# Performance work log

Hardware: AMD Instinct MI355X
Metric: run time of the kernel (lower is better)

Reference implementation:

```python
import jax, jax.numpy as jnp
import numpy as np

B, L, M, D, H, FF, W = 2, 2048, 2048, 1024, 16, 4096, 64
DH = D // H


def _layernorm(x, g, b, eps=1e-5):
    mu = x.mean(-1, keepdims=True)
    var = ((x - mu) ** 2).mean(-1, keepdims=True)
    return (x - mu) / jnp.sqrt(var + eps) * g + b


def _mha(qx, kx, wq, bq, wk, bk, wv, bv, wo, bo, mask, bias):
    Bq, Lq, _ = qx.shape
    Lk = kx.shape[1]
    q = (qx @ wq + bq).reshape(Bq, Lq, H, DH).transpose(0, 2, 1, 3)  # [B,H,Lq,DH]
    k = (kx @ wk + bk).reshape(Bq, Lk, H, DH).transpose(0, 2, 1, 3)
    v = (kx @ wv + bv).reshape(Bq, Lk, H, DH).transpose(0, 2, 1, 3)
    s = jnp.einsum('bhqd,bhkd->bhqk', q, k) / jnp.sqrt(jnp.asarray(DH, qx.dtype))
    if bias is not None:
        s = s + bias[None]  # bias: [H,Lq,Lk]
    if mask is not None:
        s = jnp.where(mask[None, None], s, jnp.asarray(-1e9, qx.dtype))
    a = jax.nn.softmax(s, axis=-1)
    o = jnp.einsum('bhqk,bhkd->bhqd', a, v).transpose(0, 2, 1, 3).reshape(Bq, Lq, D)
    return o @ wo + bo


def _forward(x, mem,
             swq, sbq, swk, sbk, swv, sbv, swo, sbo,
             cwq, cbq, cwk, cbk, cwv, cbv, cwo, cbo,
             w1, b1, w2, b2,
             g1, be1, g2, be2, g3, be3):
    i = jnp.arange(L)[:, None]
    j = jnp.arange(L)[None, :]
    # causal local window mask: attend to j<=i with i-j < W
    mask = (j <= i) & ((i - j) < W)
    # ALiBi slopes for power-of-2 head counts: 2^{-8h/H}, h=1..H
    slopes = (2.0 ** (-8.0 * jnp.arange(1, H + 1, dtype=x.dtype) / H))
    bias = slopes[:, None, None] * (j - i).astype(x.dtype)[None]  # [H,L,L], <=0 on causal part
    sa = _mha(x, x, swq, sbq, swk, sbk, swv, sbv, swo, sbo, mask, bias)
    x = _layernorm(x + sa, g1, be1)
    # cross-attn mask is all ones -> no masking, no bias
    ca = _mha(x, mem, cwq, cbq, cwk, cbk, cwv, cbv, cwo, cbo, None, None)
    x = _layernorm(x + ca, g2, be2)
    ff = jax.nn.gelu(x @ w1 + b1, approximate=False) @ w2 + b2
    return _layernorm(x + ff, g3, be3)


def setup_inputs() -> dict:
    key = jax.random.key(0)
    ks = jax.random.split(key, 16)
    s = 0.02
    inp = {
        'x': jax.random.normal(ks[0], (B, L, D), jnp.float32),
        'mem': jax.random.normal(ks[1], (B, M, D), jnp.float32),
    }
    # self-attn params
    for n, k in zip(['swq', 'swk', 'swv', 'swo'], jax.random.split(ks[2], 4)):
        inp[n] = jax.random.normal(k, (D, D), jnp.float32) * s
    for n in ['sbq', 'sbk', 'sbv', 'sbo']:
        inp[n] = jnp.zeros((D,), jnp.float32)
    # cross-attn params
    for n, k in zip(['cwq', 'cwk', 'cwv', 'cwo'], jax.random.split(ks[3], 4)):
        inp[n] = jax.random.normal(k, (D, D), jnp.float32) * s
    for n in ['cbq', 'cbk', 'cbv', 'cbo']:
        inp[n] = jnp.zeros((D,), jnp.float32)
    # FFN params
    inp['w1'] = jax.random.normal(ks[4], (D, FF), jnp.float32) * s
    inp['b1'] = jnp.zeros((FF,), jnp.float32)
    inp['w2'] = jax.random.normal(ks[5], (FF, D), jnp.float32) * s
    inp['b2'] = jnp.zeros((D,), jnp.float32)
    # LayerNorm params
    for n in ['g1', 'g2', 'g3']:
        inp[n] = jnp.ones((D,), jnp.float32)
    for n in ['be1', 'be2', 'be3']:
        inp[n] = jnp.zeros((D,), jnp.float32)
    return inp


def reference(x, mem,
              swq, sbq, swk, sbk, swv, sbv, swo, sbo,
              cwq, cbq, cwk, cbk, cwv, cbv, cwo, cbo,
              w1, b1, w2, b2,
              g1, be1, g2, be2, g3, be3):
    return _forward(x, mem,
                    swq, sbq, swk, sbk, swv, sbv, swo, sbo,
                    cwq, cbq, cwk, cbk, cwv, cbv, cwo, cbo,
                    w1, b1, w2, b2,
                    g1, be1, g2, be2, g3, be3)
```

## Files before the change

### kernel.cpp

```cpp
#include <hip/hip_runtime.h>
#include <hip/hip_bf16.h>
#include <math.h>

#define Bc 2
#define Lc 2048
#define Mc 2048
#define Dc 1024
#define Hc 16
#define FFc 4096
#define DHc 64

typedef __bf16 bf16;
typedef float f32x4 __attribute__((ext_vector_type(4)));
typedef __bf16 bf16x8 __attribute__((ext_vector_type(8)));
typedef __bf16 bf16x4 __attribute__((ext_vector_type(4)));
typedef __bf16 bf16x2 __attribute__((ext_vector_type(2)));

struct Ptrs8 { const float* p[8]; };

__device__ inline void gload16(const bf16* g, const bf16* lds_base) {
  __builtin_amdgcn_global_load_lds(
      (const __attribute__((address_space(1))) void*)g,
      (__attribute__((address_space(3))) void*)lds_base, 16, 0, 0);
}

#define WAIT_VM(n) asm volatile("s_waitcnt vmcnt(" #n ")" ::: "memory")
#define WAIT_LGKM(n) asm volatile("s_waitcnt lgkmcnt(" #n ")" ::: "memory")
#define RAW_BAR() __builtin_amdgcn_s_barrier()
#define SCHED_FENCE() __builtin_amdgcn_sched_barrier(0)

__device__ inline float gelu_f(float v) {
  float u = 0.7978845608f * (v + 0.044715f * v * v * v);
  float e = exp2f(u * 2.885390082f);
  float th = 1.0f - 2.0f / (e + 1.0f);
  return 0.5f * v * (1.0f + th);
}

__device__ inline int xcd_remap(int flat, int nwg) {
  int cpx = nwg >> 3;
  return (flat & 7) * cpx + (flat >> 3);
}

__global__ __launch_bounds__(256) void k_f2b(const float* __restrict__ in,
                                             bf16* __restrict__ out, long n4) {
  long i = (long)blockIdx.x * 256 + threadIdx.x;
  if (i >= n4) return;
  f32x4 v = *(const f32x4*)(in + i * 4);
  bf16x4 o;
  o[0] = (bf16)v[0]; o[1] = (bf16)v[1]; o[2] = (bf16)v[2]; o[3] = (bf16)v[3];
  *(bf16x4*)(out + i * 4) = o;
}

__global__ __launch_bounds__(256) void k_transpose_w8(Ptrs8 srcs,
                                                      bf16* __restrict__ out) {
  __shared__ float tile[64][65];
  const float* in = srcs.p[blockIdx.z];
  bf16* o = out + (long)blockIdx.z * Dc * Dc;
  int n0 = blockIdx.x * 64, k0 = blockIdx.y * 64;
  int t = threadIdx.x;
  int tr = t >> 4, tc = (t & 15) * 4;
#pragma unroll
  for (int p = 0; p < 4; p++) {
    int r = p * 16 + tr;
    f32x4 v = *(const f32x4*)(in + (long)(k0 + r) * Dc + n0 + tc);
    tile[r][tc] = v[0]; tile[r][tc + 1] = v[1];
    tile[r][tc + 2] = v[2]; tile[r][tc + 3] = v[3];
  }
  __syncthreads();
#pragma unroll
  for (int p = 0; p < 4; p++) {
    int rn = p * 16 + tr;
    bf16x4 ov;
    ov[0] = (bf16)tile[tc + 0][rn]; ov[1] = (bf16)tile[tc + 1][rn];
    ov[2] = (bf16)tile[tc + 2][rn]; ov[3] = (bf16)tile[tc + 3][rn];
    *(bf16x4*)(o + (long)(n0 + rn) * Dc + k0 + tc) = ov;
  }
}

__global__ __launch_bounds__(256) void k_transpose_w(const float* __restrict__ in,
                                                     bf16* __restrict__ out,
                                                     int K, int N) {
  __shared__ float tile[64][65];
  int n0 = blockIdx.x * 64, k0 = blockIdx.y * 64;
  int t = threadIdx.x;
  int tr = t >> 4, tc = (t & 15) * 4;
#pragma unroll
  for (int p = 0; p < 4; p++) {
    int r = p * 16 + tr;
    f32x4 v = *(const f32x4*)(in + (long)(k0 + r) * N + n0 + tc);
    tile[r][tc] = v[0]; tile[r][tc + 1] = v[1];
    tile[r][tc + 2] = v[2]; tile[r][tc + 3] = v[3];
  }
  __syncthreads();
#pragma unroll
  for (int p = 0; p < 4; p++) {
    int rn = p * 16 + tr;
    bf16x4 o;
    o[0] = (bf16)tile[tc + 0][rn]; o[1] = (bf16)tile[tc + 1][rn];
    o[2] = (bf16)tile[tc + 2][rn]; o[3] = (bf16)tile[tc + 3][rn];
    *(bf16x4*)(out + (long)(n0 + rn) * K + k0 + tc) = o;
  }
}

__global__ __launch_bounds__(256) void k_transpose_v(const bf16* __restrict__ vb,
                                                     bf16* __restrict__ vt, int N) {
  __shared__ bf16 tile[64][72];
  int j0 = blockIdx.x * 64;
  int bh = blockIdx.y; int b = bh >> 4; int h = bh & 15;
  int t = threadIdx.x;
#pragma unroll
  for (int c = 0; c < 2; c++) {
    int id = t + c * 256;
    int r = id >> 3, c8 = (id & 7) * 8;
    *(bf16x8*)&tile[r][c8] =
        *(const bf16x8*)(vb + ((long)(b * N + j0 + r)) * Dc + h * DHc + c8);
  }
  __syncthreads();
#pragma unroll
  for (int c = 0; c < 2; c++) {
    int id = t + c * 256;
    int d = id >> 3, j8 = (id & 7) * 8;
    bf16x8 o;
#pragma unroll
    for (int e = 0; e < 8; e++) o[e] = tile[j8 + e][d];
    *(bf16x8*)(vt + ((long)bh * DHc + d) * N + j0 + j8) = o;
  }
}

__global__ __launch_bounds__(256) void k_gemm128(
    const bf16* __restrict__ A0, const bf16* __restrict__ A1,
    const bf16* __restrict__ A2, long lda,
    const bf16* __restrict__ B0, long bstride,
    bf16* __restrict__ outB, long ldc, long cstride,
    const float* __restrict__ bias0, const float* __restrict__ bias1,
    const float* __restrict__ bias2, int Kdim, int act, float scale0) {
  __shared__ __align__(16) bf16 As[2][128 * 64];
  __shared__ __align__(16) bf16 Bs[2][128 * 64];
  int gx = gridDim.x, gy = gridDim.y;
  int nwg = gx * gy * gridDim.z;
  int flat = (blockIdx.z * gy + blockIdx.y) * gx + blockIdx.x;
  int f2 = xcd_remap(flat, nwg);
  int bxi = f2 % gx; int tmp = f2 / gx;
  int byi = tmp % gy; int z = tmp / gy;
  const bf16* A = (z == 0) ? A0 : ((z == 1) ? A1 : A2);
  const bf16* Bt = B0 + (long)z * bstride;
  const float* bias = (z == 0) ? bias0 : ((z == 1) ? bias1 : bias2);
  float scl = (z == 0) ? scale0 : 1.0f;
  long cbase = (long)z * cstride;
  int bm = byi * 128, bn = bxi * 128;
  int t = threadIdx.x, w = t >> 6, lane = t & 63;
  int wm = w >> 1, wn = w & 1;
  int lr = lane & 15, lg = lane >> 4;
  int srow = lane >> 3;
  int scol = (((lane & 7) * 16) ^ ((lane >> 3) << 4)) >> 1;
  f32x4 acc[4][4] = {};
  int nk = Kdim >> 6;
  auto stage = [&](int buf, int kt2) {
    long k0 = (long)kt2 * 64;
#pragma unroll
    for (int i = 0; i < 4; i++) {
      int row = (i * 4 + w) * 8 + srow;
      gload16(A + (long)(bm + row) * lda + k0 + scol, &As[buf][(i * 4 + w) * 512]);
      gload16(Bt + (long)(bn + row) * Kdim + k0 + scol, &Bs[buf][(i * 4 + w) * 512]);
    }
  };
  stage(0, 0);
  if (nk > 1) stage(1, 1);
  for (int kt = 0; kt < nk; ++kt) {
    int cur = kt & 1;
    if (kt + 1 < nk) { WAIT_VM(8); } else { WAIT_VM(0); }
    RAW_BAR();
    SCHED_FENCE();
    const char* pa = (const char*)&As[cur][0];
    const char* pb = (const char*)&Bs[cur][0];
    int xr = (lr & 7) << 4;
    bf16x8 af[2][4], bfr[2][4];
#pragma unroll
    for (int m = 0; m < 4; m++) {
      int row = wm * 64 + m * 16 + lr;
      af[0][m] = *(const bf16x8*)(pa + (row << 7) + ((lg * 16) ^ xr));
    }
#pragma unroll
    for (int n = 0; n < 4; n++) {
      int row = wn * 64 + n * 16 + lr;
      bfr[0][n] = *(const bf16x8*)(pb + (row << 7) + ((lg * 16) ^ xr));
    }
    SCHED_FENCE();
#pragma unroll
    for (int m = 0; m < 4; m++) {
      int row = wm * 64 + m * 16 + lr;
      af[1][m] = *(const bf16x8*)(pa + (row << 7) + ((64 + lg * 16) ^ xr));
    }
#pragma unroll
    for (int n = 0; n < 4; n++) {
      int row = wn * 64 + n * 16 + lr;
      bfr[1][n] = *(const bf16x8*)(pb + (row << 7) + ((64 + lg * 16) ^ xr));
    }
    SCHED_FENCE();
    WAIT_LGKM(8);
    SCHED_FENCE();
#pragma unroll
    for (int m = 0; m < 4; m++)
#pragma unroll
      for (int n = 0; n < 4; n++)
        acc[m][n] = __builtin_amdgcn_mfma_f32_16x16x32_bf16(af[0][m], bfr[0][n],
                                                            acc[m][n], 0, 0, 0);
    WAIT_LGKM(0);
    SCHED_FENCE();
    RAW_BAR();
    if (kt + 2 < nk) stage(cur, kt + 2);
    SCHED_FENCE();
#pragma unroll
    for (int m = 0; m < 4; m++)
#pragma unroll
      for (int n = 0; n < 4; n++)
        acc[m][n] = __builtin_amdgcn_mfma_f32_16x16x32_bf16(af[1][m], bfr[1][n],
                                                            acc[m][n], 0, 0, 0);
  }
#pragma unroll
  for (int n = 0; n < 4; n++) {
    int cg = bn + wn * 64 + n * 16 + lr;
    float bv = bias ? bias[cg] : 0.0f;
#pragma unroll
    for (int m = 0; m < 4; m++) {
#pragma unroll
      for (int rr = 0; rr < 4; rr++) {
        int rg = bm + wm * 64 + m * 16 + lg * 4 + rr;
        float v = (acc[m][n][rr] + bv) * scl;
        if (act == 1) v = gelu_f(v);
        outB[cbase + (long)rg * ldc + cg] = (bf16)v;
      }
    }
  }
}

__global__ __launch_bounds__(256) void k_gemmsk(
    const bf16* __restrict__ A, long lda,
    const bf16* __restrict__ Bt, int Kfull,
    float* __restrict__ psum, long slab, int Kchunk, int ldc) {
  __shared__ __align__(16) bf16 As[2][128 * 64];
  __shared__ __align__(16) bf16 Bs[2][128 * 64];
  int gx = gridDim.x, gy = gridDim.y;
  int nwg = gx * gy * gridDim.z;
  int flat = (blockIdx.z * gy + blockIdx.y) * gx + blockIdx.x;
  int f2 = xcd_remap(flat, nwg);
  int bxi = f2 % gx; int tmp = f2 / gx;
  int byi = tmp % gy; int z = tmp / gy;
  int bm = byi * 128, bn = bxi * 128;
  int t = threadIdx.x, w = t >> 6, lane = t & 63;
  int wm = w >> 1, wn = w & 1;
  int lr = lane & 15, lg = lane >> 4;
  int srow = lane >> 3;
  int scol = (((lane & 7) * 16) ^ ((lane >> 3) << 4)) >> 1;
  f32x4 acc[4][4] = {};
  int nk = Kchunk >> 6;
  long kstart = (long)z * Kchunk;
  auto stage = [&](int buf, int kt2) {
    long k0 = kstart + (long)kt2 * 64;
#pragma unroll
    for (int i = 0; i < 4; i++) {
      int row = (i * 4 + w) * 8 + srow;
      gload16(A + (long)(bm + row) * lda + k0 + scol, &As[buf][(i * 4 + w) * 512]);
      gload16(Bt + (long)(bn + row) * Kfull + k0 + scol, &Bs[buf][(i * 4 + w) * 512]);
    }
  };
  stage(0, 0);
  if (nk > 1) stage(1, 1);
  for (int kt = 0; kt < nk; ++kt) {
    int cur = kt & 1;
    if (kt + 1 < nk) { WAIT_VM(8); } else { WAIT_VM(0); }
    RAW_BAR();
    SCHED_FENCE();
    const char* pa = (const char*)&As[cur][0];
    const char* pb = (const char*)&Bs[cur][0];
    int xr = (lr & 7) << 4;
    bf16x8 af[2][4], bfr[2][4];
#pragma unroll
    for (int m = 0; m < 4; m++) {
      int row = wm * 64 + m * 16 + lr;
      af[0][m] = *(const bf16x8*)(pa + (row << 7) + ((lg * 16) ^ xr));
    }
#pragma unroll
    for (int n = 0; n < 4; n++) {
      int row = wn * 64 + n * 16 + lr;
      bfr[0][n] = *(const bf16x8*)(pb + (row << 7) + ((lg * 16) ^ xr));
    }
    SCHED_FENCE();
#pragma unroll
    for (int m = 0; m < 4; m++) {
      int row = wm * 64 + m * 16 + lr;
      af[1][m] = *(const bf16x8*)(pa + (row << 7) + ((64 + lg * 16) ^ xr));
    }
#pragma unroll
    for (int n = 0; n < 4; n++) {
      int row = wn * 64 + n * 16 + lr;
      bfr[1][n] = *(const bf16x8*)(pb + (row << 7) + ((64 + lg * 16) ^ xr));
    }
    SCHED_FENCE();
    WAIT_LGKM(8);
    SCHED_FENCE();
#pragma unroll
    for (int m = 0; m < 4; m++)
#pragma unroll
      for (int n = 0; n < 4; n++)
        acc[m][n] = __builtin_amdgcn_mfma_f32_16x16x32_bf16(af[0][m], bfr[0][n],
                                                            acc[m][n], 0, 0, 0);
    WAIT_LGKM(0);
    SCHED_FENCE();
    RAW_BAR();
    if (kt + 2 < nk) stage(cur, kt + 2);
    SCHED_FENCE();
#pragma unroll
    for (int m = 0; m < 4; m++)
#pragma unroll
      for (int n = 0; n < 4; n++)
        acc[m][n] = __builtin_amdgcn_mfma_f32_16x16x32_bf16(af[1][m], bfr[1][n],
                                                            acc[m][n], 0, 0, 0);
  }
  float* po = psum + (long)z * slab;
#pragma unroll
  for (int n = 0; n < 4; n++) {
    int cg = bn + wn * 64 + n * 16 + lr;
#pragma unroll
    for (int m = 0; m < 4; m++) {
#pragma unroll
      for (int rr = 0; rr < 4; rr++) {
        int rg = bm + wm * 64 + m * 16 + lg * 4 + rr;
        po[(long)rg * ldc + cg] = acc[m][n][rr];
      }
    }
  }
}

template <int WINDOWED>
__global__ __launch_bounds__(256) void k_flash(const bf16* __restrict__ Qg,
                                               const bf16* __restrict__ Kg,
                                               const bf16* __restrict__ Vtg,
                                               bf16* __restrict__ Og, int nkv) {
  __shared__ __align__(16) bf16 Qs[64 * 64];
  __shared__ __align__(16) bf16 Ks[2][64 * 64];
  __shared__ __align__(16) bf16 Vs[2][64 * 64];
  int flat = blockIdx.y * 32 + blockIdx.x;
  int flat2 = (flat & 7) * 128 + (flat >> 3);
  int i0 = (flat2 & 31) * 64;
  int bh = flat2 >> 5;
  int b = bh >> 4, h = bh & 15;
  int t = threadIdx.x, w = t >> 6, lane = t & 63;
  int lr = lane & 15, lg = lane >> 4;
  long qoff = ((long)b * Lc + i0) * Dc + h * DHc;
  long koff = ((long)b * nkv) * Dc + h * DHc;
  long vtoff = (long)bh * DHc * nkv;
  int o0 = w * 1024 + (lane << 4), o1 = o0 + 4096;
  int r0 = o0 >> 7, c0 = (o0 & 127) ^ ((r0 & 7) << 4);
  int r1 = o1 >> 7, c1 = (o1 & 127) ^ ((r1 & 7) << 4);
  int d0 = c0 >> 1, d1 = c1 >> 1;
  gload16(Qg + qoff + (long)r0 * Dc + d0, &Qs[w * 512]);
  gload16(Qg + qoff + (long)r1 * Dc + d1, &Qs[2048 + w * 512]);
  int kb0 = WINDOWED ? (i0 >= 64 ? i0 - 64 : 0) : 0;
  int nt = WINDOWED ? ((i0 - kb0) >> 6) + 1 : (nkv >> 6);
  auto stage = [&](int buf, int kbase) {
    gload16(Kg + koff + (long)(kbase + r0) * Dc + d0, &Ks[buf][w * 512]);
    gload16(Kg + koff + (long)(kbase + r1) * Dc + d1, &Ks[buf][2048 + w * 512]);
    gload16(Vtg + vtoff + (long)r0 * nkv + kbase + d0, &Vs[buf][w * 512]);
    gload16(Vtg + vtoff + (long)r1 * nkv + kbase + d1, &Vs[buf][2048 + w * 512]);
  };
  stage(0, kb0);
  WAIT_VM(4);
  RAW_BAR();
  SCHED_FENCE();
  bf16x8 bq[2];
#pragma unroll
  for (int ks = 0; ks < 2; ks++) {
    int rq = w * 16 + lr, cb = ks * 64 + lg * 16;
    bq[ks] = *(const bf16x8*)&Qs[((rq << 7) + (cb ^ ((rq & 7) << 4))) >> 1];
  }
  char* pbase = (char*)&Qs[w * 1024];
  float mrun = -1e30f, lrun = 0.f;
  f32x4 oa[4] = {};
  float slopeL2 = WINDOWED ? exp2f(-0.5f * (float)(h + 1)) * 1.44269504f : 0.0f;
  int qabs = i0 + w * 16 + lr;
  for (int tch = 0; tch < nt; tch++) {
    int cur = tch & 1;
    if (tch + 1 < nt) {
      stage(cur ^ 1, kb0 + (tch + 1) * 64);
      WAIT_VM(4);
    } else {
      WAIT_VM(0);
    }
    RAW_BAR();
    SCHED_FENCE();
    int kbase = kb0 + tch * 64;
    f32x4 st[4] = {};
    __builtin_amdgcn_s_setprio(1);
#pragma unroll
    for (int ks = 0; ks < 2; ks++) {
#pragma unroll
      for (int m = 0; m < 4; m++) {
        int rk = m * 16 + lr, cb = ks * 64 + lg * 16;
        bf16x8 ka = *(const bf16x8*)&Ks[cur][((rk << 7) + (cb ^ ((rk & 7) << 4))) >> 1];
        st[m] = __builtin_amdgcn_mfma_f32_16x16x32_bf16(ka, bq[ks], st[m], 0, 0, 0);
      }
    }
    __builtin_amdgcn_s_setprio(0);
    float sc[4][4];
#pragma unroll
    for (int m = 0; m < 4; m++)
#pragma unroll
      for (int rr = 0; rr < 4; rr++) {
        float v = st[m][rr];
        if (WINDOWED) {
          int kab = kbase + m * 16 + lg * 4 + rr;
          v += slopeL2 * (float)(kab - qabs);
          bool valid = (kab <= qabs) && (qabs - kab < 64);
          v = valid ? v : -3.0e38f;
        }
        sc[m][rr] = v;
      }
    float pmax = fmaxf(fmaxf(sc[0][0], sc[0][1]), sc[0][2]);
    pmax = fmaxf(fmaxf(pmax, sc[0][3]), sc[1][0]);
    pmax = fmaxf(fmaxf(pmax, sc[1][1]), sc[1][2]);
    pmax = fmaxf(fmaxf(pmax, sc[1][3]), sc[2][0]);
    pmax = fmaxf(fmaxf(pmax, sc[2][1]), sc[2][2]);
    pmax = fmaxf(fmaxf(pmax, sc[2][3]), sc[3][0]);
    pmax = fmaxf(fmaxf(pmax, sc[3][1]), sc[3][2]);
    pmax = fmaxf(pmax, sc[3][3]);
    pmax = fmaxf(pmax, __shfl_xor(pmax, 16));
    pmax = fmaxf(pmax, __shfl_xor(pmax, 32));
    float mx = mrun;
    if (!__all(pmax - mrun <= 8.0f)) {
      mx = fmaxf(mrun, pmax);
      float corr = exp2f(mrun - mx);
      mrun = mx;
      lrun *= corr;
      float cq[4];
#pragma unroll
      for (int rr = 0; rr < 4; rr++) cq[rr] = __shfl(corr, lg * 4 + rr);
#pragma unroll
      for (int jd = 0; jd < 4; jd++) {
        oa[jd][0] *= cq[0]; oa[jd][1] *= cq[1];
        oa[jd][2] *= cq[2]; oa[jd][3] *= cq[3];
      }
    }
    float ps0 = 0.f, ps1 = 0.f;
#pragma unroll
    for (int m = 0; m < 4; m++) {
#pragma unroll
      for (int hh = 0; hh < 2; hh++) {
        float p0 = exp2f(sc[m][2 * hh] - mx);
        float p1 = exp2f(sc[m][2 * hh + 1] - mx);
        ps0 += p0; ps1 += p1;
        bf16x2 pw; pw[0] = (bf16)p0; pw[1] = (bf16)p1;
        int kcol = m * 16 + lg * 4 + 2 * hh;
        *(bf16x2*)(pbase + (lr << 7) + (((kcol << 1)) ^ ((lr & 7) << 4))) = pw;
      }
    }
    lrun += ps0 + ps1;
    __builtin_amdgcn_s_setprio(1);
#pragma unroll
    for (int ks = 0; ks < 2; ks++) {
      bf16x8 pa = *(const bf16x8*)(pbase + (lr << 7) +
                                   (((ks * 64 + lg * 16)) ^ ((lr & 7) << 4)));
#pragma unroll
      for (int jd = 0; jd < 4; jd++) {
        int rv = jd * 16 + lr, cb = ks * 64 + lg * 16;
        bf16x8 vf = *(const bf16x8*)&Vs[cur][((rv << 7) + (cb ^ ((rv & 7) << 4))) >> 1];
        oa[jd] = __builtin_amdgcn_mfma_f32_16x16x32_bf16(pa, vf, oa[jd], 0, 0, 0);
      }
    }
    __builtin_amdgcn_s_setprio(0);
    WAIT_LGKM(0);
    SCHED_FENCE();
    RAW_BAR();
  }
  float ls = lrun + __shfl_xor(lrun, 16);
  ls += __shfl_xor(ls, 32);
  float inv = 1.0f / ls;
  float iq[4];
#pragma unroll
  for (int rr = 0; rr < 4; rr++) iq[rr] = __shfl(inv, lg * 4 + rr);
#pragma unroll
  for (int rr = 0; rr < 4; rr++) {
    int qo = i0 + w * 16 + lg * 4 + rr;
#pragma unroll
    for (int jd = 0; jd < 4; jd++)
      Og[((long)b * Lc + qo) * Dc + h * DHc + jd * 16 + lr] =
          (bf16)(oa[jd][rr] * iq[rr]);
  }
}

template <int NS>
__global__ __launch_bounds__(256) void k_lnred(const float* __restrict__ psum,
                                               long slab,
                                               const float* __restrict__ bias,
                                               const float* __restrict__ addsrc,
                                               const float* __restrict__ g,
                                               const float* __restrict__ bb,
                                               float* __restrict__ outF,
                                               bf16* __restrict__ outB) {
  long row = blockIdx.x;
  int t = threadIdx.x; int lane = t & 63; int wid = t >> 6;
  __shared__ float red[8];
  f32x4 v = *(const f32x4*)(psum + row * Dc + t * 4);
#pragma unroll
  for (int s = 1; s < NS; s++) {
    f32x4 u = *(const f32x4*)(psum + s * slab + row * Dc + t * 4);
    v[0] += u[0]; v[1] += u[1]; v[2] += u[2]; v[3] += u[3];
  }
  f32x4 bv = *(const f32x4*)(bias + t * 4);
  f32x4 av = *(const f32x4*)(addsrc + row * Dc + t * 4);
  v[0] += bv[0] + av[0]; v[1] += bv[1] + av[1];
  v[2] += bv[2] + av[2]; v[3] += bv[3] + av[3];
  float s = v[0] + v[1] + v[2] + v[3];
  float s2 = v[0] * v[0] + v[1] * v[1] + v[2] * v[2] + v[3] * v[3];
#pragma unroll
  for (int off = 1; off < 64; off <<= 1) {
    s += __shfl_xor(s, off);
    s2 += __shfl_xor(s2, off);
  }
  if (lane == 0) { red[wid] = s; red[4 + wid] = s2; }
  __syncthreads();
  s = red[0] + red[1] + red[2] + red[3];
  s2 = red[4] + red[5] + red[6] + red[7];
  float mu = s * (1.0f / Dc);
  float var = s2 * (1.0f / Dc) - mu * mu;
  float rs = rsqrtf(var + 1e-5f);
#pragma unroll
  for (int e = 0; e < 4; e++) {
    int c = t * 4 + e;
    float y = (v[e] - mu) * rs * g[c] + bb[c];
    if (outF) outF[row * Dc + c] = y;
    if (outB) outB[row * Dc + c] = (bf16)y;
  }
}

extern "C" void kernel_launch(void* const* d_in, const int* in_sizes, int n_in,
                              void* d_out, int out_size, void* d_ws,
                              size_t ws_size, hipStream_t stream) {
  (void)in_sizes; (void)n_in; (void)out_size; (void)ws_size;
  const float* x = (const float*)d_in[0];
  const float* mem = (const float*)d_in[1];
  const float* swq = (const float*)d_in[2];
  const float* swk = (const float*)d_in[3];
  const float* swv = (const float*)d_in[4];
  const float* swo = (const float*)d_in[5];
  const float* sbq = (const float*)d_in[6];
  const float* sbk = (const float*)d_in[7];
  const float* sbv = (const float*)d_in[8];
  const float* sbo = (const float*)d_in[9];
  const float* cwq = (const float*)d_in[10];
  const float* cwk = (const float*)d_in[11];
  const float* cwv = (const float*)d_in[12];
  const float* cwo = (const float*)d_in[13];
  const float* cbq = (const float*)d_in[14];
  const float* cbk = (const float*)d_in[15];
  const float* cbv = (const float*)d_in[16];
  const float* cbo = (const float*)d_in[17];
  const float* w1 = (const float*)d_in[18];
  const float* b1 = (const float*)d_in[19];
  const float* w2 = (const float*)d_in[20];
  const float* b2 = (const float*)d_in[21];
  const float* g1 = (const float*)d_in[22];
  const float* g2 = (const float*)d_in[23];
  const float* g3 = (const float*)d_in[24];
  const float* be1 = (const float*)d_in[25];
  const float* be2 = (const float*)d_in[26];
  const float* be3 = (const float*)d_in[27];
  float* out = (float*)d_out;

  char* ws = (char*)d_ws;
  size_t off = 0;
  auto alloc = [&](size_t bytes) -> char* {
    char* p = ws + off;
    off = (off + bytes + 255) & ~(size_t)255;
    return p;
  };

  const long BL = (long)Bc * Lc;
  const long BM = (long)Bc * Mc;
  const long DD = (long)Dc * Dc;
  const long SL = BL * Dc;
  const float QSCL = 0.125f * 1.44269504f;

  bf16* wT0 = (bf16*)alloc((size_t)8 * DD * 2);
  bf16* w1T = (bf16*)alloc((size_t)FFc * Dc * 2);
  bf16* w2T = (bf16*)alloc((size_t)Dc * FFc * 2);
  bf16* xb = (bf16*)alloc((size_t)BL * Dc * 2);
  bf16* memb = (bf16*)alloc((size_t)BM * Dc * 2);
  bf16* x1b = (bf16*)alloc((size_t)BL * Dc * 2);
  bf16* x2b = (bf16*)alloc((size_t)BL * Dc * 2);
  bf16* qb = (bf16*)alloc((size_t)BL * Dc * 2);
  bf16* kb = (bf16*)alloc((size_t)BM * Dc * 2);
  bf16* vb = (bf16*)alloc((size_t)BM * Dc * 2);
  bf16* ob = (bf16*)alloc((size_t)BL * Dc * 2);
  bf16* vtS = (bf16*)alloc((size_t)Bc * Hc * DHc * Lc * 2);
  bf16* vtC = (bf16*)alloc((size_t)Bc * Hc * DHc * Mc * 2);
  float* x1f = (float*)alloc((size_t)BL * Dc * 4);
  float* x2f = (float*)alloc((size_t)BL * Dc * 4);
  bf16* ffh = (bf16*)alloc((size_t)BL * FFc * 2);
  float* psum = (float*)alloc((size_t)4 * SL * 4);

  Ptrs8 srcs;
  srcs.p[0] = swq; srcs.p[1] = swk; srcs.p[2] = swv; srcs.p[3] = swo;
  srcs.p[4] = cwq; srcs.p[5] = cwk; srcs.p[6] = cwv; srcs.p[7] = cwo;
  k_transpose_w8<<<dim3(Dc / 64, Dc / 64, 8), 256, 0, stream>>>(srcs, wT0);
  k_transpose_w<<<dim3(FFc / 64, Dc / 64), 256, 0, stream>>>(w1, w1T, Dc, FFc);
  k_transpose_w<<<dim3(Dc / 64, FFc / 64), 256, 0, stream>>>(w2, w2T, FFc, Dc);
  k_f2b<<<dim3((unsigned)(BL * Dc / 4 / 256)), 256, 0, stream>>>(x, xb, BL * Dc / 4);
  k_f2b<<<dim3((unsigned)(BM * Dc / 4 / 256)), 256, 0, stream>>>(mem, memb, BM * Dc / 4);

  k_gemm128<<<dim3(Dc / 128, BL / 128, 3), 256, 0, stream>>>(
      xb, xb, xb, Dc, wT0, DD, qb, Dc, SL, sbq, sbk, sbv, Dc, 0, QSCL);
  k_transpose_v<<<dim3(Lc / 64, Bc * Hc), 256, 0, stream>>>(vb, vtS, Lc);
  k_flash<1><<<dim3(Lc / 64, Bc * Hc), 256, 0, stream>>>(qb, kb, vtS, ob, Lc);
  k_gemmsk<<<dim3(Dc / 128, BL / 128, 2), 256, 0, stream>>>(
      ob, Dc, wT0 + 3 * DD, Dc, psum, SL, 512, Dc);
  k_lnred<2><<<dim3((unsigned)BL), 256, 0, stream>>>(psum, SL, sbo, x, g1, be1,
                                                     x1f, x1b);

  k_gemm128<<<dim3(Dc / 128, BM / 128, 3), 256, 0, stream>>>(
      x1b, memb, memb, Dc, wT0 + 4 * DD, DD, qb, Dc, SL, cbq, cbk, cbv, Dc, 0, QSCL);
  k_transpose_v<<<dim3(Mc / 64, Bc * Hc), 256, 0, stream>>>(vb, vtC, Mc);
  k_flash<0><<<dim3(Lc / 64, Bc * Hc), 256, 0, stream>>>(qb, kb, vtC, ob, Mc);
  k_gemmsk<<<dim3(Dc / 128, BL / 128, 2), 256, 0, stream>>>(
      ob, Dc, wT0 + 7 * DD, Dc, psum, SL, 512, Dc);
  k_lnred<2><<<dim3((unsigned)BL), 256, 0, stream>>>(psum, SL, cbo, x1f, g2, be2,
                                                     x2f, x2b);

  k_gemm128<<<dim3(FFc / 128, BL / 128, 1), 256, 0, stream>>>(
      x2b, x2b, x2b, Dc, w1T, 0, ffh, FFc, 0, b1, b1, b1, Dc, 1, 1.0f);
  k_gemmsk<<<dim3(Dc / 128, BL / 128, 4), 256, 0, stream>>>(
      ffh, FFc, w2T, FFc, psum, SL, 1024, Dc);
  k_lnred<4><<<dim3((unsigned)BL), 256, 0, stream>>>(psum, SL, b2, x2f, g3, be3,
                                                     out, nullptr);
}
```

Measured before the change: 383.4 us.

## Use fixed-max softmax with MFMA row sums in cross-attention; bf16 split-K partials

For non-windowed cross-attention, the running max is fixed from the first KV tile, replacing per-tile max reduction and rescaling. Row sums are computed with an MFMA against a ones vector, and a rare overflow guard rescales when sums grow large. Split-K partial sums are stored in bf16 instead of fp32, halving that traffic into the layernorm reduction at the cost of precision. The P stores are also widened to bf16x4.

```diff
diff --git a/kernel.cpp b/kernel.cpp
--- a/kernel.cpp
+++ b/kernel.cpp
@@ -237,7 +237,7 @@
 __global__ __launch_bounds__(256) void k_gemmsk(
     const bf16* __restrict__ A, long lda,
     const bf16* __restrict__ Bt, int Kfull,
-    float* __restrict__ psum, long slab, int Kchunk, int ldc) {
+    bf16* __restrict__ psum, long slab, int Kchunk, int ldc) {
   __shared__ __align__(16) bf16 As[2][128 * 64];
   __shared__ __align__(16) bf16 Bs[2][128 * 64];
   int gx = gridDim.x, gy = gridDim.y;
@@ -317,7 +317,7 @@
         acc[m][n] = __builtin_amdgcn_mfma_f32_16x16x32_bf16(af[1][m], bfr[1][n],
                                                             acc[m][n], 0, 0, 0);
   }
-  float* po = psum + (long)z * slab;
+  bf16* po = psum + (long)z * slab;
 #pragma unroll
   for (int n = 0; n < 4; n++) {
     int cg = bn + wn * 64 + n * 16 + lr;
@@ -326,7 +326,7 @@
 #pragma unroll
       for (int rr = 0; rr < 4; rr++) {
         int rg = bm + wm * 64 + m * 16 + lg * 4 + rr;
-        po[(long)rg * ldc + cg] = acc[m][n][rr];
+        po[(long)rg * ldc + cg] = (bf16)acc[m][n][rr];
       }
     }
   }
@@ -376,9 +376,15 @@
   }
   char* pbase = (char*)&Qs[w * 1024];
   float mrun = -1e30f, lrun = 0.f;
+  float mx_c = 0.0f;
   f32x4 oa[4] = {};
+  f32x4 lacc = {};
+  bf16x8 ones;
+#pragma unroll
+  for (int e = 0; e < 8; e++) ones[e] = (bf16)1.0f;
   float slopeL2 = WINDOWED ? exp2f(-0.5f * (float)(h + 1)) * 1.44269504f : 0.0f;
   int qabs = i0 + w * 16 + lr;
+  int xr16 = (lr & 7) << 4;
   for (int tch = 0; tch < nt; tch++) {
     int cur = tch & 1;
     if (tch + 1 < nt) {
@@ -402,94 +408,147 @@
       }
     }
     __builtin_amdgcn_s_setprio(0);
-    float sc[4][4];
-#pragma unroll
-    for (int m = 0; m < 4; m++)
-#pragma unroll
-      for (int rr = 0; rr < 4; rr++) {
-        float v = st[m][rr];
-        if (WINDOWED) {
+    if (WINDOWED) {
+      float sc[4][4];
+#pragma unroll
+      for (int m = 0; m < 4; m++)
+#pragma unroll
+        for (int rr = 0; rr < 4; rr++) {
+          float v = st[m][rr];
           int kab = kbase + m * 16 + lg * 4 + rr;
           v += slopeL2 * (float)(kab - qabs);
           bool valid = (kab <= qabs) && (qabs - kab < 64);
-          v = valid ? v : -3.0e38f;
+          sc[m][rr] = valid ? v : -3.0e38f;
         }
-        sc[m][rr] = v;
-      }
-    float pmax = fmaxf(fmaxf(sc[0][0], sc[0][1]), sc[0][2]);
-    pmax = fmaxf(fmaxf(pmax, sc[0][3]), sc[1][0]);
-    pmax = fmaxf(fmaxf(pmax, sc[1][1]), sc[1][2]);
-    pmax = fmaxf(fmaxf(pmax, sc[1][3]), sc[2][0]);
-    pmax = fmaxf(fmaxf(pmax, sc[2][1]), sc[2][2]);
-    pmax = fmaxf(fmaxf(pmax, sc[2][3]), sc[3][0]);
-    pmax = fmaxf(fmaxf(pmax, sc[3][1]), sc[3][2]);
-    pmax = fmaxf(pmax, sc[3][3]);
-    pmax = fmaxf(pmax, __shfl_xor(pmax, 16));
-    pmax = fmaxf(pmax, __shfl_xor(pmax, 32));
-    float mx = mrun;
-    if (!__all(pmax - mrun <= 8.0f)) {
-      mx = fmaxf(mrun, pmax);
-      float corr = exp2f(mrun - mx);
-      mrun = mx;
-      lrun *= corr;
-      float cq[4];
-#pragma unroll
-      for (int rr = 0; rr < 4; rr++) cq[rr] = __shfl(corr, lg * 4 + rr);
-#pragma unroll
-      for (int jd = 0; jd < 4; jd++) {
-        oa[jd][0] *= cq[0]; oa[jd][1] *= cq[1];
-        oa[jd][2] *= cq[2]; oa[jd][3] *= cq[3];
-      }
-    }
-    float ps0 = 0.f, ps1 = 0.f;
-#pragma unroll
-    for (int m = 0; m < 4; m++) {
-#pragma unroll
-      for (int hh = 0; hh < 2; hh++) {
-        float p0 = exp2f(sc[m][2 * hh] - mx);
-        float p1 = exp2f(sc[m][2 * hh + 1] - mx);
-        ps0 += p0; ps1 += p1;
-        bf16x2 pw; pw[0] = (bf16)p0; pw[1] = (bf16)p1;
-        int kcol = m * 16 + lg * 4 + 2 * hh;
-        *(bf16x2*)(pbase + (lr << 7) + (((kcol << 1)) ^ ((lr & 7) << 4))) = pw;
-      }
-    }
-    lrun += ps0 + ps1;
-    __builtin_amdgcn_s_setprio(1);
-#pragma unroll
-    for (int ks = 0; ks < 2; ks++) {
-      bf16x8 pa = *(const bf16x8*)(pbase + (lr << 7) +
-                                   (((ks * 64 + lg * 16)) ^ ((lr & 7) << 4)));
-#pragma unroll
-      for (int jd = 0; jd < 4; jd++) {
-        int rv = jd * 16 + lr, cb = ks * 64 + lg * 16;
-        bf16x8 vf = *(const bf16x8*)&Vs[cur][((rv << 7) + (cb ^ ((rv & 7) << 4))) >> 1];
-        oa[jd] = __builtin_amdgcn_mfma_f32_16x16x32_bf16(pa, vf, oa[jd], 0, 0, 0);
-      }
-    }
-    __builtin_amdgcn_s_setprio(0);
+      float pmax = sc[0][0];
+#pragma unroll
+      for (int m = 0; m < 4; m++)
+#pragma unroll
+        for (int rr = 0; rr < 4; rr++) pmax = fmaxf(pmax, sc[m][rr]);
+      pmax = fmaxf(pmax, __shfl_xor(pmax, 16));
+      pmax = fmaxf(pmax, __shfl_xor(pmax, 32));
+      float mx = mrun;
+      if (!__all(pmax - mrun <= 8.0f)) {
+        mx = fmaxf(mrun, pmax);
+        float corr = exp2f(mrun - mx);
+        mrun = mx;
+        lrun *= corr;
+        float cq[4];
+#pragma unroll
+        for (int rr = 0; rr < 4; rr++) cq[rr] = __shfl(corr, lg * 4 + rr);
+#pragma unroll
+        for (int jd = 0; jd < 4; jd++) {
+          oa[jd][0] *= cq[0]; oa[jd][1] *= cq[1];
+          oa[jd][2] *= cq[2]; oa[jd][3] *= cq[3];
+        }
+      }
+      float ps = 0.f;
+#pragma unroll
+      for (int m = 0; m < 4; m++) {
+        float p0 = exp2f(sc[m][0] - mx);
+        float p1 = exp2f(sc[m][1] - mx);
+        float p2 = exp2f(sc[m][2] - mx);
+        float p3 = exp2f(sc[m][3] - mx);
+        ps += (p0 + p1) + (p2 + p3);
+        bf16x4 pw; pw[0] = (bf16)p0; pw[1] = (bf16)p1;
+        pw[2] = (bf16)p2; pw[3] = (bf16)p3;
+        *(bf16x4*)(pbase + (lr << 7) + ((m * 32 + lg * 8) ^ xr16)) = pw;
+      }
+      lrun += ps;
+      __builtin_amdgcn_s_setprio(1);
+#pragma unroll
+      for (int ks = 0; ks < 2; ks++) {
+        bf16x8 pa = *(const bf16x8*)(pbase + (lr << 7) +
+                                     ((ks * 64 + lg * 16) ^ xr16));
+#pragma unroll
+        for (int jd = 0; jd < 4; jd++) {
+          int rv = jd * 16 + lr, cb = ks * 64 + lg * 16;
+          bf16x8 vf = *(const bf16x8*)&Vs[cur][((rv << 7) + (cb ^ ((rv & 7) << 4))) >> 1];
+          oa[jd] = __builtin_amdgcn_mfma_f32_16x16x32_bf16(pa, vf, oa[jd], 0, 0, 0);
+        }
+      }
+      __builtin_amdgcn_s_setprio(0);
+    } else {
+      if (tch == 0) {
+        float pmax = st[0][0];
+#pragma unroll
+        for (int m = 0; m < 4; m++)
+#pragma unroll
+          for (int rr = 0; rr < 4; rr++) pmax = fmaxf(pmax, st[m][rr]);
+        pmax = fmaxf(pmax, __shfl_xor(pmax, 16));
+        pmax = fmaxf(pmax, __shfl_xor(pmax, 32));
+        mx_c = pmax;
+      }
+#pragma unroll
+      for (int m = 0; m < 4; m++) {
+        float p0 = exp2f(st[m][0] - mx_c);
+        float p1 = exp2f(st[m][1] - mx_c);
+        float p2 = exp2f(st[m][2] - mx_c);
+        float p3 = exp2f(st[m][3] - mx_c);
+        bf16x4 pw; pw[0] = (bf16)p0; pw[1] = (bf16)p1;
+        pw[2] = (bf16)p2; pw[3] = (bf16)p3;
+        *(bf16x4*)(pbase + (lr << 7) + ((m * 32 + lg * 8) ^ xr16)) = pw;
+      }
+      __builtin_amdgcn_s_setprio(1);
+#pragma unroll
+      for (int ks = 0; ks < 2; ks++) {
+        bf16x8 pa = *(const bf16x8*)(pbase + (lr << 7) +
+                                     ((ks * 64 + lg * 16) ^ xr16));
+        lacc = __builtin_amdgcn_mfma_f32_16x16x32_bf16(pa, ones, lacc, 0, 0, 0);
+#pragma unroll
+        for (int jd = 0; jd < 4; jd++) {
+          int rv = jd * 16 + lr, cb = ks * 64 + lg * 16;
+          bf16x8 vf = *(const bf16x8*)&Vs[cur][((rv << 7) + (cb ^ ((rv & 7) << 4))) >> 1];
+          oa[jd] = __builtin_amdgcn_mfma_f32_16x16x32_bf16(pa, vf, oa[jd], 0, 0, 0);
+        }
+      }
+      __builtin_amdgcn_s_setprio(0);
+      float lm = fmaxf(fmaxf(lacc[0], lacc[1]), fmaxf(lacc[2], lacc[3]));
+      if (!__all(lm < 16777216.0f)) {
+        const float cs = 2.3283064365386963e-10f;
+        mx_c += 32.0f;
+#pragma unroll
+        for (int jd = 0; jd < 4; jd++) {
+          oa[jd][0] *= cs; oa[jd][1] *= cs;
+          oa[jd][2] *= cs; oa[jd][3] *= cs;
+        }
+        lacc[0] *= cs; lacc[1] *= cs; lacc[2] *= cs; lacc[3] *= cs;
+      }
+    }
     WAIT_LGKM(0);
     SCHED_FENCE();
     RAW_BAR();
   }
-  float ls = lrun + __shfl_xor(lrun, 16);
-  ls += __shfl_xor(ls, 32);
-  float inv = 1.0f / ls;
-  float iq[4];
-#pragma unroll
-  for (int rr = 0; rr < 4; rr++) iq[rr] = __shfl(inv, lg * 4 + rr);
-#pragma unroll
-  for (int rr = 0; rr < 4; rr++) {
-    int qo = i0 + w * 16 + lg * 4 + rr;
-#pragma unroll
-    for (int jd = 0; jd < 4; jd++)
-      Og[((long)b * Lc + qo) * Dc + h * DHc + jd * 16 + lr] =
-          (bf16)(oa[jd][rr] * iq[rr]);
+  if (WINDOWED) {
+    float ls = lrun + __shfl_xor(lrun, 16);
+    ls += __shfl_xor(ls, 32);
+    float inv = 1.0f / ls;
+    float iq[4];
+#pragma unroll
+    for (int rr = 0; rr < 4; rr++) iq[rr] = __shfl(inv, lg * 4 + rr);
+#pragma unroll
+    for (int rr = 0; rr < 4; rr++) {
+      int qo = i0 + w * 16 + lg * 4 + rr;
+#pragma unroll
+      for (int jd = 0; jd < 4; jd++)
+        Og[((long)b * Lc + qo) * Dc + h * DHc + jd * 16 + lr] =
+            (bf16)(oa[jd][rr] * iq[rr]);
+    }
+  } else {
+#pragma unroll
+    for (int rr = 0; rr < 4; rr++) {
+      float inv = 1.0f / lacc[rr];
+      int qo = i0 + w * 16 + lg * 4 + rr;
+#pragma unroll
+      for (int jd = 0; jd < 4; jd++)
+        Og[((long)b * Lc + qo) * Dc + h * DHc + jd * 16 + lr] =
+            (bf16)(oa[jd][rr] * inv);
+    }
   }
 }
 
 template <int NS>
-__global__ __launch_bounds__(256) void k_lnred(const float* __restrict__ psum,
+__global__ __launch_bounds__(256) void k_lnred(const bf16* __restrict__ psum,
                                                long slab,
                                                const float* __restrict__ bias,
                                                const float* __restrict__ addsrc,
@@ -500,11 +559,13 @@
   long row = blockIdx.x;
   int t = threadIdx.x; int lane = t & 63; int wid = t >> 6;
   __shared__ float red[8];
-  f32x4 v = *(const f32x4*)(psum + row * Dc + t * 4);
+  bf16x4 v0 = *(const bf16x4*)(psum + row * Dc + t * 4);
+  float v[4] = {(float)v0[0], (float)v0[1], (float)v0[2], (float)v0[3]};
 #pragma unroll
   for (int s = 1; s < NS; s++) {
-    f32x4 u = *(const f32x4*)(psum + s * slab + row * Dc + t * 4);
-    v[0] += u[0]; v[1] += u[1]; v[2] += u[2]; v[3] += u[3];
+    bf16x4 u = *(const bf16x4*)(psum + s * slab + row * Dc + t * 4);
+    v[0] += (float)u[0]; v[1] += (float)u[1];
+    v[2] += (float)u[2]; v[3] += (float)u[3];
   }
   f32x4 bv = *(const f32x4*)(bias + t * 4);
   f32x4 av = *(const f32x4*)(addsrc + row * Dc + t * 4);
@@ -597,7 +658,7 @@
   float* x1f = (float*)alloc((size_t)BL * Dc * 4);
   float* x2f = (float*)alloc((size_t)BL * Dc * 4);
   bf16* ffh = (bf16*)alloc((size_t)BL * FFc * 2);
-  float* psum = (float*)alloc((size_t)4 * SL * 4);
+  bf16* psum = (bf16*)alloc((size_t)4 * SL * 2);
 
   Ptrs8 srcs;
   srcs.p[0] = swq; srcs.p[1] = swk; srcs.p[2] = swv; srcs.p[3] = swo;
```

Result: faster. 359.9 us (-6.1%).
